# Performance work log

Measured on AMD Instinct MI355X. Metric: run time of the kernel, lower is better.

## Reference

```python
import jax, jax.numpy as jnp
import numpy as np

# Dropout (p=0.5) is treated as identity (eval mode) for a deterministic reference.

def setup_inputs() -> dict:
    key = jax.random.key(0)
    k1, k2, k3, k4 = jax.random.split(key, 4)
    S, B, NIN, NHID = 512, 64, 256, 512
    inp = jax.random.normal(k1, (S, B, NIN), dtype=jnp.float32)
    W = jax.random.normal(k2, (NIN, 4 * NHID), dtype=jnp.float32) * 0.02
    U = jax.random.normal(k3, (NHID, 4 * NHID), dtype=jnp.float32) * 0.02
    b = jax.random.normal(k4, (4 * NHID,), dtype=jnp.float32) * 0.02
    return {"input": inp, "W": W, "U": U, "b": b}


def reference(input, W, U, b):
    nhid = U.shape[0]
    batch = input.shape[1]
    # Precompute input projection for all timesteps: [S, B, 4H]
    xW = jnp.einsum('sbi,ih->sbh', input, W) + b

    def step(carry, xw_t):
        h, c = carry
        gates = xw_t + h @ U  # [B, 4H]
        i = jax.nn.sigmoid(gates[:, :nhid])
        f = jax.nn.sigmoid(gates[:, nhid:2 * nhid])
        g = jnp.tanh(gates[:, 2 * nhid:3 * nhid])
        o = jax.nn.sigmoid(gates[:, 3 * nhid:])
        c_new = f * c + i * g
        h_new = o * jnp.tanh(c_new)
        return (h_new, c_new), h_new

    h0 = jnp.zeros((batch, nhid), dtype=input.dtype)
    c0 = jnp.zeros((batch, nhid), dtype=input.dtype)
    (h_t, c_t), output = jax.lax.scan(step, (h0, c0), xW)
    return output, h_t, c_t
```

## Files before the change

kernel.cpp:

```cpp
#include <hip/hip_runtime.h>

#define NBLK 64
#define NTHR 256
#define SEQ  512
#define BAT  64
#define NINP 256
#define NHID 512
#define LDG  2048

typedef __attribute__((ext_vector_type(8))) short short8;
typedef __attribute__((ext_vector_type(4))) float f32x4;

static __device__ __forceinline__ unsigned short f2bf(float x) {
    return __builtin_bit_cast(unsigned short, (__bf16)x);
}
static __device__ __forceinline__ float sigm(float x)  { return 1.0f / (1.0f + __expf(-x)); }
static __device__ __forceinline__ float tanh_(float x) { return 2.0f / (1.0f + __expf(-2.0f * x)) - 1.0f; }

static __device__ __forceinline__ void hload(short8& d, const unsigned short* p) {
    asm volatile("global_load_dwordx4 %0, %1, off sc0 sc1" : "=v"(d) : "v"(p) : "memory");
}
static __device__ __forceinline__ void hstore16(short8 v, unsigned short* p) {
    asm volatile("global_store_dwordx4 %0, %1, off sc0 sc1" :: "v"(p), "v"(v) : "memory");
}
static __device__ __forceinline__ void pload(f32x4& d, const float* p) {
    asm volatile("global_load_dwordx4 %0, %1, off" : "=v"(d) : "v"(p) : "memory");
}

__global__ __launch_bounds__(NTHR, 1)
void lstm_persistent(const float* __restrict__ x, const float* __restrict__ W,
                     const float* __restrict__ U, const float* __restrict__ bias,
                     float* __restrict__ out, char* __restrict__ wsB)
{
    __shared__ short8 lds_s[4 * 16];

    const int bk   = blockIdx.x;
    const int tid  = threadIdx.x;
    const int w    = tid >> 6;
    const int lane = tid & 63;
    const int c16  = lane & 15;
    const int rq   = lane >> 4;

    unsigned int*   flags = (unsigned int*)wsB;
    unsigned short* hbuf  = (unsigned short*)(wsB + 16384);

    const int col0 = (c16 >> 3) * NHID + (c16 & 7) + bk * 8;
    const int col1 = col0 + 2 * NHID;

    short8 ut[2][16];
#pragma unroll
    for (int kb = 0; kb < 16; ++kb) {
        const int k0 = kb * 32 + rq * 8;
        short8 v0, v1;
#pragma unroll
        for (int j = 0; j < 8; ++j) {
            v0[j] = (short)f2bf(U[(size_t)(k0 + j) * LDG + col0]);
            v1[j] = (short)f2bf(U[(size_t)(k0 + j) * LDG + col1]);
        }
        ut[0][kb] = v0; ut[1][kb] = v1;
    }
    short8 wt[2][8];
#pragma unroll
    for (int kb = 0; kb < 8; ++kb) {
        const int k0 = kb * 32 + rq * 8;
        short8 v0, v1;
#pragma unroll
        for (int j = 0; j < 8; ++j) {
            v0[j] = (short)f2bf(W[(size_t)(k0 + j) * LDG + col0]);
            v1[j] = (short)f2bf(W[(size_t)(k0 + j) * LDG + col1]);
        }
        wt[0][kb] = v0; wt[1][kb] = v1;
    }
    const float bias0 = bias[col0];
    const float bias1 = bias[col1];

    const int  arow  = w * 16 + c16;
    const bool lower = (c16 < 8);
    const bool up    = (c16 & 8);
    const int  hcol  = bk * 8 + (c16 & 7);
    float cst[4] = {0.f, 0.f, 0.f, 0.f};

    float* hout  = out + (size_t)SEQ * BAT * NHID;
    float* cout_ = hout + BAT * NHID;

    unsigned short* lds_w = (unsigned short*)&lds_s[w * 16];

    f32x4 accA[2][4];
#pragma unroll
    for (int nt = 0; nt < 2; ++nt)
#pragma unroll
        for (int ch = 0; ch < 4; ++ch) accA[nt][ch] = (f32x4){0.f, 0.f, 0.f, 0.f};
    {
        const float* xr = x + (size_t)arow * NINP + rq * 8;
#pragma unroll
        for (int kb = 0; kb < 8; ++kb) {
            f32x4 a0 = *(const f32x4*)(xr + kb * 32);
            f32x4 a1 = *(const f32x4*)(xr + kb * 32 + 4);
            short8 v;
#pragma unroll
            for (int j = 0; j < 4; ++j) {
                v[j]     = (short)f2bf(a0[j]);
                v[j + 4] = (short)f2bf(a1[j]);
            }
            const int ch = kb & 3;
            accA[0][ch] = __builtin_amdgcn_mfma_f32_16x16x32_bf16(v, wt[0][kb], accA[0][ch], 0, 0, 0);
            accA[1][ch] = __builtin_amdgcn_mfma_f32_16x16x32_bf16(v, wt[1][kb], accA[1][ch], 0, 0, 0);
        }
    }

    f32x4 xraw[16];

    for (int t = 0; t < SEQ; ++t) {
        const int pR = (t + 1) & 1;
        const int pW = t & 1;

        if (t < SEQ - 1) {
            const float* xr = x + ((size_t)(t + 1) * BAT + arow) * NINP + rq * 8;
#pragma unroll
            for (int kb = 0; kb < 8; ++kb) {
                pload(xraw[2 * kb],     xr + kb * 32);
                pload(xraw[2 * kb + 1], xr + kb * 32 + 4);
            }
        }

        if (t > 0) {
            {
                const unsigned int* fp = flags + (lane * 4 + w) * 16;
                unsigned f;
                do {
                    asm volatile("global_load_dword %0, %1, off sc0 sc1\n\t"
                                 "s_waitcnt vmcnt(0)"
                                 : "=v"(f) : "v"(fp) : "memory");
                } while (!__all(f >= (unsigned)t));
            }
            __builtin_amdgcn_sched_barrier(0);

            const unsigned short* rb = hbuf + pR * 32768 + arow * 8;
            short8 hreg[16];
#pragma unroll
            for (int kb = 0; kb < 16; ++kb)
                hload(hreg[kb], rb + (kb * 4 + rq) * 512);
            asm volatile("s_waitcnt vmcnt(0)" ::: "memory");
            __builtin_amdgcn_sched_barrier(0);
#pragma unroll
            for (int kb = 0; kb < 16; ++kb) {
                const int ch = kb & 3;
                accA[0][ch] = __builtin_amdgcn_mfma_f32_16x16x32_bf16(hreg[kb], ut[0][kb], accA[0][ch], 0, 0, 0);
                accA[1][ch] = __builtin_amdgcn_mfma_f32_16x16x32_bf16(hreg[kb], ut[1][kb], accA[1][ch], 0, 0, 0);
            }
        }

        f32x4 gif = accA[0][0] + accA[0][1] + accA[0][2] + accA[0][3];
        f32x4 ggo = accA[1][0] + accA[1][1] + accA[1][2] + accA[1][3];
#pragma unroll
        for (int j = 0; j < 4; ++j) { gif[j] += bias0; ggo[j] += bias1; }

        f32x4 oif, ogo;
#pragma unroll
        for (int j = 0; j < 4; ++j) {
            oif[j] = __shfl_xor(gif[j], 8, 64);
            ogo[j] = __shfl_xor(ggo[j], 8, 64);
        }
        float hv[4];
#pragma unroll
        for (int j = 0; j < 4; ++j) {
            const float gi = up ? oif[j] : gif[j];
            const float gf = up ? gif[j] : oif[j];
            const float gg = up ? ogo[j] : ogo[j] * 0.0f + (up ? ogo[j] : ggo[j]);
            const float go = 0.0f;
            (void)gg; (void)go;
            break;
        }
#pragma unroll
        for (int j = 0; j < 4; ++j) {
            const float gi = up ? oif[j] : gif[j];
            const float gf = up ? gif[j] : oif[j];
            const float gg = up ? ogo[j] : ggo[j];
            const float go = up ? ggo[j] : ogo[j];
            const float iv = sigm(gi);
            const float fv = sigm(gf);
            const float gv = tanh_(gg);
            const float ov = sigm(go);
            const float cn = fv * cst[j] + iv * gv;
            cst[j] = cn;
            hv[j] = ov * tanh_(cn);
        }

        if (t < SEQ - 1) {
            if (lower) {
#pragma unroll
                for (int j = 0; j < 4; ++j)
                    lds_w[(rq * 4 + j) * 8 + c16] = f2bf(hv[j]);
            }
            if (lane < 16) {
                short8 hpk = lds_s[w * 16 + lane];
                hstore16(hpk, hbuf + pW * 32768 + bk * 512 + (size_t)(w * 16 + lane) * 8);
            }
            __builtin_amdgcn_sched_barrier(0);

            if (t == 0) {
                asm volatile("s_waitcnt vmcnt(0)" ::: "memory");
            }
            __builtin_amdgcn_sched_barrier(0);
#pragma unroll
            for (int i = 0; i < 16; ++i)
                asm volatile("" : "+v"(xraw[i]));

#pragma unroll
            for (int nt = 0; nt < 2; ++nt)
#pragma unroll
                for (int ch = 0; ch < 4; ++ch) accA[nt][ch] = (f32x4){0.f, 0.f, 0.f, 0.f};
#pragma unroll
            for (int kb = 0; kb < 8; ++kb) {
                short8 v;
#pragma unroll
                for (int j = 0; j < 4; ++j) {
                    v[j]     = (short)f2bf(xraw[2 * kb][j]);
                    v[j + 4] = (short)f2bf(xraw[2 * kb + 1][j]);
                }
                const int ch = kb & 3;
                accA[0][ch] = __builtin_amdgcn_mfma_f32_16x16x32_bf16(v, wt[0][kb], accA[0][ch], 0, 0, 0);
                accA[1][ch] = __builtin_amdgcn_mfma_f32_16x16x32_bf16(v, wt[1][kb], accA[1][ch], 0, 0, 0);
            }
            __builtin_amdgcn_sched_barrier(0);

            asm volatile("s_waitcnt vmcnt(0)" ::: "memory");
            if (lane == 0) {
                unsigned int* fp2 = flags + (bk * 4 + w) * 16;
                unsigned int val = (unsigned)(t + 1);
                asm volatile("global_store_dword %0, %1, off sc0 sc1"
                             :: "v"(fp2), "v"(val) : "memory");
            }

            if (lower) {
#pragma unroll
                for (int j = 0; j < 4; ++j) {
                    const int batch = w * 16 + rq * 4 + j;
                    out[((size_t)t * BAT + batch) * NHID + hcol] = hv[j];
                }
            }
        } else {
            if (lower) {
#pragma unroll
                for (int j = 0; j < 4; ++j) {
                    const int batch = w * 16 + rq * 4 + j;
                    out[((size_t)t * BAT + batch) * NHID + hcol] = hv[j];
                    hout[batch * NHID + hcol]  = hv[j];
                    cout_[batch * NHID + hcol] = cst[j];
                }
            }
        }
    }
}

extern "C" void kernel_launch(void* const* d_in, const int* in_sizes, int n_in,
                              void* d_out, int out_size, void* d_ws, size_t ws_size,
                              hipStream_t stream) {
    (void)in_sizes; (void)n_in; (void)out_size; (void)ws_size;
    const float* x  = (const float*)d_in[0];
    const float* W  = (const float*)d_in[1];
    const float* U  = (const float*)d_in[2];
    const float* b  = (const float*)d_in[3];
    float* out = (float*)d_out;

    (void)hipMemsetAsync(d_ws, 0, 16384, stream);
    hipLaunchKernelGGL(lstm_persistent, dim3(NBLK), dim3(NTHR), 0, stream,
                       x, W, U, b, out, (char*)d_ws);
}
```

Measured before the change: 2.230 ms.

## Pipeline flag polling and defer next-step input loads behind h loads

Makes the flag spin-wait double-buffered, so a new flag load is issued before the previous one is checked, which shortens the polling latency on the inter-block barrier. The x prefetch for the next timestep moves to after the h loads, and the wait is now vmcnt(16), so the MFMAs on h can start while the x loads are still outstanding. Dead code is also removed. The hand-counted vmcnt values are fragile and could produce ordering bugs if the count of outstanding loads is wrong.

```diff
diff --git a/kernel.cpp b/kernel.cpp
--- a/kernel.cpp
+++ b/kernel.cpp
@@ -114,24 +114,21 @@
         const int pR = (t + 1) & 1;
         const int pW = t & 1;
 
-        if (t < SEQ - 1) {
-            const float* xr = x + ((size_t)(t + 1) * BAT + arow) * NINP + rq * 8;
-#pragma unroll
-            for (int kb = 0; kb < 8; ++kb) {
-                pload(xraw[2 * kb],     xr + kb * 32);
-                pload(xraw[2 * kb + 1], xr + kb * 32 + 4);
-            }
-        }
-
         if (t > 0) {
+            asm volatile("s_waitcnt vmcnt(0)" ::: "memory");
+
+            unsigned fA, fB;
             {
                 const unsigned int* fp = flags + (lane * 4 + w) * 16;
-                unsigned f;
-                do {
-                    asm volatile("global_load_dword %0, %1, off sc0 sc1\n\t"
-                                 "s_waitcnt vmcnt(0)"
-                                 : "=v"(f) : "v"(fp) : "memory");
-                } while (!__all(f >= (unsigned)t));
+                asm volatile("global_load_dword %0, %1, off sc0 sc1" : "=v"(fA) : "v"(fp) : "memory");
+                for (;;) {
+                    asm volatile("global_load_dword %0, %1, off sc0 sc1" : "=v"(fB) : "v"(fp) : "memory");
+                    asm volatile("s_waitcnt vmcnt(1)" : "+v"(fA) :: "memory");
+                    if (__all(fA >= (unsigned)t)) break;
+                    asm volatile("global_load_dword %0, %1, off sc0 sc1" : "=v"(fA) : "v"(fp) : "memory");
+                    asm volatile("s_waitcnt vmcnt(1)" : "+v"(fB) :: "memory");
+                    if (__all(fB >= (unsigned)t)) break;
+                }
             }
             __builtin_amdgcn_sched_barrier(0);
 
@@ -140,7 +137,18 @@
 #pragma unroll
             for (int kb = 0; kb < 16; ++kb)
                 hload(hreg[kb], rb + (kb * 4 + rq) * 512);
-            asm volatile("s_waitcnt vmcnt(0)" ::: "memory");
+            if (t < SEQ - 1) {
+                const float* xr = x + ((size_t)(t + 1) * BAT + arow) * NINP + rq * 8;
+#pragma unroll
+                for (int kb = 0; kb < 8; ++kb) {
+                    pload(xraw[2 * kb],     xr + kb * 32);
+                    pload(xraw[2 * kb + 1], xr + kb * 32 + 4);
+                }
+                asm volatile("s_waitcnt vmcnt(16)" ::: "memory");
+            } else {
+                asm volatile("s_waitcnt vmcnt(0)" ::: "memory");
+            }
+            asm volatile("" :: "v"(fA), "v"(fB));
             __builtin_amdgcn_sched_barrier(0);
 #pragma unroll
             for (int kb = 0; kb < 16; ++kb) {
@@ -148,6 +156,13 @@
                 accA[0][ch] = __builtin_amdgcn_mfma_f32_16x16x32_bf16(hreg[kb], ut[0][kb], accA[0][ch], 0, 0, 0);
                 accA[1][ch] = __builtin_amdgcn_mfma_f32_16x16x32_bf16(hreg[kb], ut[1][kb], accA[1][ch], 0, 0, 0);
             }
+        } else {
+            const float* xr = x + ((size_t)BAT + arow) * NINP + rq * 8;
+#pragma unroll
+            for (int kb = 0; kb < 8; ++kb) {
+                pload(xraw[2 * kb],     xr + kb * 32);
+                pload(xraw[2 * kb + 1], xr + kb * 32 + 4);
+            }
         }
 
         f32x4 gif = accA[0][0] + accA[0][1] + accA[0][2] + accA[0][3];
@@ -162,15 +177,6 @@
             ogo[j] = __shfl_xor(ggo[j], 8, 64);
         }
         float hv[4];
-#pragma unroll
-        for (int j = 0; j < 4; ++j) {
-            const float gi = up ? oif[j] : gif[j];
-            const float gf = up ? gif[j] : oif[j];
-            const float gg = up ? ogo[j] : ogo[j] * 0.0f + (up ? ogo[j] : ggo[j]);
-            const float go = 0.0f;
-            (void)gg; (void)go;
-            break;
-        }
 #pragma unroll
         for (int j = 0; j < 4; ++j) {
             const float gi = up ? oif[j] : gif[j];
@@ -196,11 +202,7 @@
                 short8 hpk = lds_s[w * 16 + lane];
                 hstore16(hpk, hbuf + pW * 32768 + bk * 512 + (size_t)(w * 16 + lane) * 8);
             }
-            __builtin_amdgcn_sched_barrier(0);
-
-            if (t == 0) {
-                asm volatile("s_waitcnt vmcnt(0)" ::: "memory");
-            }
+            asm volatile("s_waitcnt vmcnt(1)" ::: "memory");
             __builtin_amdgcn_sched_barrier(0);
 #pragma unroll
             for (int i = 0; i < 16; ++i)
```

Measured after the change: 3.448 ms. 54.6% more time.
